# Kernel tuning notes

Measured on AMD Instinct MI355X. Metric: run time of the kernel, lower is better.

Reference implementation:

```python
import jax, jax.numpy as jnp
import numpy as np

BETA = 0.25


def setup_inputs() -> dict:
    key = jax.random.key(0)
    k1, k2 = jax.random.split(key)
    z = jax.random.normal(k1, (16, 64, 64, 64), dtype=jnp.float32)        # [B, e_dim, H, W]
    codebook = jax.random.normal(k2, (2048, 64), dtype=jnp.float32)       # [n_e, e_dim]
    return {"z": z, "codebook": codebook}


def reference(z, codebook):
    B, C, H, W = z.shape
    n_e = codebook.shape[0]
    sg = jax.lax.stop_gradient

    zp = jnp.transpose(z, (0, 2, 3, 1))                # [B, H, W, C]
    zf = zp.reshape(-1, C)                             # [N, C]

    # nearest-code logits (inner product; CE in source is dead code)
    logits = zf @ codebook.T                           # [N, n_e]
    idx = jnp.argmax(logits, axis=1)                   # [N]

    z_q = codebook[idx].reshape(zp.shape)              # [B, H, W, C]

    # commitment + codebook loss (this overwrites the CE loss in the source)
    loss = BETA * jnp.mean((sg(z_q) - zp) ** 2) + jnp.mean((z_q - sg(zp)) ** 2)

    # straight-through estimator
    z_q_st = zp + sg(z_q - zp)

    # perplexity via one-hot mean (scatter-add instead of dense one-hot)
    counts = jnp.zeros((n_e,), dtype=zp.dtype).at[idx].add(1.0)
    e_mean = counts / idx.shape[0]
    perplexity = jnp.exp(-jnp.sum(e_mean * jnp.log(e_mean + 1e-10)))

    indices = idx.reshape(B, H * W).astype(jnp.int32)
    z_q_out = jnp.transpose(z_q_st, (0, 3, 1, 2))      # back to [B, C, H, W]
    return z_q_out, loss, perplexity, indices
```

## Files before the change

kernel.cpp:

```cpp
#include <hip/hip_runtime.h>

#define C_DIM   64
#define HW      4096
#define NROWS   65536
#define N_E     2048
#define N_ELEM  4194304
#define OUT_LOSS_OFF 4194304
#define OUT_PPL_OFF  4194305
#define OUT_IDX_OFF  4194306

#define ROWS_B   128
#define NTILE    (N_E / 16)
#define TILE_U   384

typedef __attribute__((ext_vector_type(8))) short bf16x8;
typedef __attribute__((ext_vector_type(4))) float f32x4;

__device__ __forceinline__ unsigned short f2bf(float f) {
    unsigned u = __float_as_uint(f);
    return (unsigned short)((u + 0x7FFFu + ((u >> 16) & 1u)) >> 16);
}
__device__ __forceinline__ float bf2f(unsigned short b) {
    return __uint_as_float(((unsigned)b) << 16);
}

__global__ __launch_bounds__(256) void vq_prep(
    const float* __restrict__ cb, unsigned short* __restrict__ cbp,
    int* __restrict__ counts, float* __restrict__ loss_accum)
{
    const int u = blockIdx.x * 256 + threadIdx.x;
    if (u < N_E) counts[u] = 0;
    if (u == 0)  *loss_accum = 0.f;
    const int c = u >> 6, k = u & 63;
    const float v = cb[u];
    const unsigned short s1 = f2bf(v);
    const float r1 = v - bf2f(s1);
    const unsigned short s2 = f2bf(r1);
    const float r2 = r1 - bf2f(s2);
    const unsigned short s3 = f2bf(r2);
    const int tile = c >> 4, k2 = k >> 5, kk = k & 31;
    const int lane = (kk >> 3) * 16 + (c & 15), i = kk & 7;
    const int base = ((tile * 3 + 0) * 2 + k2) * 512 + lane * 8 + i;
    cbp[base]        = s1;
    cbp[base + 1024] = s2;
    cbp[base + 2048] = s3;
}

#define M16(A_, B_, C_) __builtin_amdgcn_mfma_f32_16x16x32_bf16((A_), (B_), (C_), 0, 0, 0)

#define PASS8(AA, ACC, NT)                                                      \
    ACC = M16(AA[0], zf[0][NT][0], ACC); ACC = M16(AA[1], zf[0][NT][1], ACC);   \
    ACC = M16(AA[0], zf[1][NT][0], ACC); ACC = M16(AA[1], zf[1][NT][1], ACC);   \
    ACC = M16(AA[2], zf[0][NT][0], ACC); ACC = M16(AA[3], zf[0][NT][1], ACC);   \
    ACC = M16(AA[2], zf[1][NT][0], ACC); ACC = M16(AA[3], zf[1][NT][1], ACC);   \
    ACC = M16(AA[0], zf[2][NT][0], ACC); ACC = M16(AA[1], zf[2][NT][1], ACC);   \
    ACC = M16(AA[4], zf[0][NT][0], ACC); ACC = M16(AA[5], zf[0][NT][1], ACC);   \
    ACC = M16(AA[2], zf[2][NT][0], ACC); ACC = M16(AA[3], zf[2][NT][1], ACC);   \
    ACC = M16(AA[4], zf[1][NT][0], ACC); ACC = M16(AA[5], zf[1][NT][1], ACC);

#define COMPUTE_TILE(T_, AA)                                                    \
    {                                                                           \
        f32x4 acc0 = zero4, acc1 = zero4;                                       \
        PASS8(AA, acc0, 0)                                                      \
        PASS8(AA, acc1, 1)                                                      \
        const int cbase = (T_) * 16 + lg * 4;                                   \
        _Pragma("unroll")                                                       \
        for (int r = 0; r < 4; ++r) {                                           \
            if (acc0[r] > best0) { best0 = acc0[r]; bi0 = cbase + r; }          \
            if (acc1[r] > best1) { best1 = acc1[r]; bi1 = cbase + r; }          \
        }                                                                       \
    }

__global__ __launch_bounds__(256, 2) void vq_mfma(
    const float* __restrict__ z, const float* __restrict__ cb,
    const unsigned short* __restrict__ cbp, float* __restrict__ out,
    int* __restrict__ counts, float* __restrict__ loss_accum)
{
    __shared__ int   sidx[ROWS_B];
    __shared__ float wsum[4];

    const int tid  = threadIdx.x;
    const int lane = tid & 63;
    const int wv   = tid >> 6;
    const int l15  = lane & 15, lg = lane >> 4;
    const int row0 = blockIdx.x * ROWS_B;
    const int b    = row0 >> 12;
    const int hw0  = row0 & 4095;
    const float* zb = z + (size_t)b * C_DIM * HW + hw0;

    bf16x8 zf[3][2][2];
#pragma unroll
    for (int nt = 0; nt < 2; ++nt) {
        const int row_l = wv * 32 + nt * 16 + l15;
#pragma unroll
        for (int k2 = 0; k2 < 2; ++k2) {
#pragma unroll
            for (int i = 0; i < 8; ++i) {
                float v = zb[(size_t)(k2 * 32 + lg * 8 + i) * HW + row_l];
                unsigned short s1 = f2bf(v);
                float r1 = v - bf2f(s1);
                unsigned short s2 = f2bf(r1);
                float r2 = r1 - bf2f(s2);
                zf[0][nt][k2][i] = (short)s1;
                zf[1][nt][k2][i] = (short)s2;
                zf[2][nt][k2][i] = (short)f2bf(r2);
            }
        }
    }

    const bf16x8* cbpf = (const bf16x8*)cbp;
    float best0 = -3.4e38f, best1 = -3.4e38f;
    int   bi0 = 0, bi1 = 0;
    const f32x4 zero4 = {0.f, 0.f, 0.f, 0.f};

    bf16x8 Acur[6], Anxt[6];
#pragma unroll
    for (int f = 0; f < 6; ++f) Acur[f] = cbpf[f * 64 + lane];

#pragma unroll 1
    for (int t = 0; t < NTILE; t += 2) {
#pragma unroll
        for (int f = 0; f < 6; ++f)
            Anxt[f] = cbpf[(size_t)(t + 1) * TILE_U + f * 64 + lane];

        COMPUTE_TILE(t, Acur)

        if (t + 2 < NTILE) {
#pragma unroll
            for (int f = 0; f < 6; ++f)
                Acur[f] = cbpf[(size_t)(t + 2) * TILE_U + f * 64 + lane];
        }

        COMPUTE_TILE(t + 1, Anxt)
    }

#pragma unroll
    for (int off = 16; off <= 32; off <<= 1) {
        float ob; int oi;
        ob = __shfl_xor(best0, off, 64); oi = __shfl_xor(bi0, off, 64);
        if (ob > best0 || (ob == best0 && oi < bi0)) { best0 = ob; bi0 = oi; }
        ob = __shfl_xor(best1, off, 64); oi = __shfl_xor(bi1, off, 64);
        if (ob > best1 || (ob == best1 && oi < bi1)) { best1 = ob; bi1 = oi; }
    }
    if (lane < 32) {
        const int nt = lane >> 4;
        const int row_l = wv * 32 + lane;
        const int ii = (nt == 0) ? bi0 : bi1;
        sidx[row_l] = ii;
        out[OUT_IDX_OFF + row0 + row_l] = (float)ii;
        atomicAdd(&counts[ii], 1);
    }
    __syncthreads();

    float* ob0 = out + (size_t)b * C_DIM * HW + hw0;
    float lsum = 0.f;
#pragma unroll
    for (int j = 0; j < 8; ++j) {
        const int m = j * 256 + tid;
        const int r = m & 127, c4 = m >> 7;
        const float4 q4 = *(const float4*)(cb + (size_t)sidx[r] * C_DIM + c4 * 4);
#pragma unroll
        for (int q = 0; q < 4; ++q) {
            const int c = c4 * 4 + q;
            const float zv = zb[(size_t)c * HW + r];
            const float qv = (q == 0) ? q4.x : (q == 1) ? q4.y : (q == 2) ? q4.z : q4.w;
            const float d = qv - zv;
            lsum += d * d;
            ob0[(size_t)c * HW + r] = zv + d;
        }
    }
    for (int off = 32; off > 0; off >>= 1) lsum += __shfl_down(lsum, off, 64);
    if (lane == 0) wsum[wv] = lsum;
    __syncthreads();
    if (tid == 0)
        atomicAdd(loss_accum, wsum[0] + wsum[1] + wsum[2] + wsum[3]);
}

__global__ __launch_bounds__(256) void vq_finalize(
    const int* __restrict__ counts, const float* __restrict__ loss_accum,
    float* __restrict__ out)
{
    float h = 0.f;
    for (int e = threadIdx.x; e < N_E; e += 256) {
        float em = (float)counts[e] * (1.0f / (float)NROWS);
        h -= em * logf(em + 1e-10f);
    }
    for (int off = 32; off > 0; off >>= 1) h += __shfl_down(h, off, 64);
    __shared__ float hs[4];
    const int lane = threadIdx.x & 63, w = threadIdx.x >> 6;
    if (lane == 0) hs[w] = h;
    __syncthreads();
    if (threadIdx.x == 0) {
        float H = hs[0] + hs[1] + hs[2] + hs[3];
        float m = loss_accum[0] * (1.0f / (float)N_ELEM);
        out[OUT_LOSS_OFF] = 0.25f * m + m;
        out[OUT_PPL_OFF]  = expf(H);
    }
}

extern "C" void kernel_launch(void* const* d_in, const int* in_sizes, int n_in,
                              void* d_out, int out_size, void* d_ws, size_t ws_size,
                              hipStream_t stream)
{
    const float* z  = (const float*)d_in[0];
    const float* cb = (const float*)d_in[1];
    float* out = (float*)d_out;

    int*            counts     = (int*)d_ws;
    float*          loss_accum = (float*)((char*)d_ws + N_E * sizeof(int));
    unsigned short* cbp        = (unsigned short*)((char*)d_ws + 16384);

    vq_prep<<<N_E * C_DIM / 256, 256, 0, stream>>>(cb, cbp, counts, loss_accum);
    vq_mfma<<<NROWS / ROWS_B, 256, 0, stream>>>(z, cb, cbp, out, counts, loss_accum);
    vq_finalize<<<1, 256, 0, stream>>>(counts, loss_accum, out);
}
```

Before: 170.1 us.

## Split codebook across wave pairs and fuse finalize into last block

Each wave now handles 64 rows against half the codebook (1024 codes) instead of 32 rows against all 2048 codes. This doubles reuse of each loaded codebook fragment per MFMA and halves per-wave codebook traffic. The two halves are merged through shared memory. The separate finalize kernel is removed and replaced by a last-block-done atomic counter, saving a launch. In exchange, the z fragments and accumulators use more registers, which may reduce occupancy.

```diff
diff --git a/kernel.cpp b/kernel.cpp
--- a/kernel.cpp
+++ b/kernel.cpp
@@ -10,7 +10,8 @@
 #define OUT_IDX_OFF  4194306
 
 #define ROWS_B   128
-#define NTILE    (N_E / 16)
+#define NBLOCKS  (NROWS / ROWS_B)
+#define NTILE_W  64
 #define TILE_U   384
 
 typedef __attribute__((ext_vector_type(8))) short bf16x8;
@@ -26,11 +27,12 @@
 
 __global__ __launch_bounds__(256) void vq_prep(
     const float* __restrict__ cb, unsigned short* __restrict__ cbp,
-    int* __restrict__ counts, float* __restrict__ loss_accum)
+    int* __restrict__ counts, float* __restrict__ loss_accum,
+    int* __restrict__ done)
 {
     const int u = blockIdx.x * 256 + threadIdx.x;
     if (u < N_E) counts[u] = 0;
-    if (u == 0)  *loss_accum = 0.f;
+    if (u == 0)  { *loss_accum = 0.f; *done = 0; }
     const int c = u >> 6, k = u & 63;
     const float v = cb[u];
     const unsigned short s1 = f2bf(v);
@@ -60,38 +62,50 @@
 
 #define COMPUTE_TILE(T_, AA)                                                    \
     {                                                                           \
-        f32x4 acc0 = zero4, acc1 = zero4;                                       \
+        f32x4 acc0 = zero4, acc1 = zero4, acc2 = zero4, acc3 = zero4;           \
         PASS8(AA, acc0, 0)                                                      \
         PASS8(AA, acc1, 1)                                                      \
-        const int cbase = (T_) * 16 + lg * 4;                                   \
+        PASS8(AA, acc2, 2)                                                      \
+        PASS8(AA, acc3, 3)                                                      \
+        const int cbase = ch * 1024 + (T_) * 16 + lg * 4;                       \
         _Pragma("unroll")                                                       \
         for (int r = 0; r < 4; ++r) {                                           \
             if (acc0[r] > best0) { best0 = acc0[r]; bi0 = cbase + r; }          \
             if (acc1[r] > best1) { best1 = acc1[r]; bi1 = cbase + r; }          \
+            if (acc2[r] > best2) { best2 = acc2[r]; bi2 = cbase + r; }          \
+            if (acc3[r] > best3) { best3 = acc3[r]; bi3 = cbase + r; }          \
         }                                                                       \
     }
 
 __global__ __launch_bounds__(256, 2) void vq_mfma(
     const float* __restrict__ z, const float* __restrict__ cb,
     const unsigned short* __restrict__ cbp, float* __restrict__ out,
-    int* __restrict__ counts, float* __restrict__ loss_accum)
+    int* __restrict__ counts, float* __restrict__ loss_accum,
+    int* __restrict__ done)
 {
+    __shared__ float sbest[2][ROWS_B];
+    __shared__ int   sbi[2][ROWS_B];
     __shared__ int   sidx[ROWS_B];
     __shared__ float wsum[4];
+    __shared__ int   slast;
 
     const int tid  = threadIdx.x;
     const int lane = tid & 63;
     const int wv   = tid >> 6;
     const int l15  = lane & 15, lg = lane >> 4;
+    const int rh   = wv >> 1;
+    const int ch   = wv & 1;
     const int row0 = blockIdx.x * ROWS_B;
     const int b    = row0 >> 12;
     const int hw0  = row0 & 4095;
     const float* zb = z + (size_t)b * C_DIM * HW + hw0;
 
-    bf16x8 zf[3][2][2];
-#pragma unroll
-    for (int nt = 0; nt < 2; ++nt) {
-        const int row_l = wv * 32 + nt * 16 + l15;
+    if (tid == 0) slast = 0;
+
+    bf16x8 zf[3][4][2];
+#pragma unroll
+    for (int nt = 0; nt < 4; ++nt) {
+        const int row_l = rh * 64 + nt * 16 + l15;
 #pragma unroll
         for (int k2 = 0; k2 < 2; ++k2) {
 #pragma unroll
@@ -108,9 +122,9 @@
         }
     }
 
-    const bf16x8* cbpf = (const bf16x8*)cbp;
-    float best0 = -3.4e38f, best1 = -3.4e38f;
-    int   bi0 = 0, bi1 = 0;
+    const bf16x8* cbpf = (const bf16x8*)cbp + (size_t)ch * NTILE_W * TILE_U;
+    float best0 = -3.4e38f, best1 = -3.4e38f, best2 = -3.4e38f, best3 = -3.4e38f;
+    int   bi0 = 0, bi1 = 0, bi2 = 0, bi3 = 0;
     const f32x4 zero4 = {0.f, 0.f, 0.f, 0.f};
 
     bf16x8 Acur[6], Anxt[6];
@@ -118,14 +132,14 @@
     for (int f = 0; f < 6; ++f) Acur[f] = cbpf[f * 64 + lane];
 
 #pragma unroll 1
-    for (int t = 0; t < NTILE; t += 2) {
+    for (int t = 0; t < NTILE_W; t += 2) {
 #pragma unroll
         for (int f = 0; f < 6; ++f)
             Anxt[f] = cbpf[(size_t)(t + 1) * TILE_U + f * 64 + lane];
 
         COMPUTE_TILE(t, Acur)
 
-        if (t + 2 < NTILE) {
+        if (t + 2 < NTILE_W) {
 #pragma unroll
             for (int f = 0; f < 6; ++f)
                 Acur[f] = cbpf[(size_t)(t + 2) * TILE_U + f * 64 + lane];
@@ -141,13 +155,24 @@
         if (ob > best0 || (ob == best0 && oi < bi0)) { best0 = ob; bi0 = oi; }
         ob = __shfl_xor(best1, off, 64); oi = __shfl_xor(bi1, off, 64);
         if (ob > best1 || (ob == best1 && oi < bi1)) { best1 = ob; bi1 = oi; }
-    }
-    if (lane < 32) {
-        const int nt = lane >> 4;
-        const int row_l = wv * 32 + lane;
-        const int ii = (nt == 0) ? bi0 : bi1;
-        sidx[row_l] = ii;
-        out[OUT_IDX_OFF + row0 + row_l] = (float)ii;
+        ob = __shfl_xor(best2, off, 64); oi = __shfl_xor(bi2, off, 64);
+        if (ob > best2 || (ob == best2 && oi < bi2)) { best2 = ob; bi2 = oi; }
+        ob = __shfl_xor(best3, off, 64); oi = __shfl_xor(bi3, off, 64);
+        if (ob > best3 || (ob == best3 && oi < bi3)) { best3 = ob; bi3 = oi; }
+    }
+    {
+        float bb = (lg == 0) ? best0 : (lg == 1) ? best1 : (lg == 2) ? best2 : best3;
+        int   ii = (lg == 0) ? bi0   : (lg == 1) ? bi1   : (lg == 2) ? bi2   : bi3;
+        sbest[ch][rh * 64 + lane] = bb;
+        sbi[ch][rh * 64 + lane]   = ii;
+    }
+    __syncthreads();
+    if (tid < ROWS_B) {
+        float b0 = sbest[0][tid], b1 = sbest[1][tid];
+        int   i0 = sbi[0][tid],   i1 = sbi[1][tid];
+        const int ii = (b1 > b0) ? i1 : i0;
+        sidx[tid] = ii;
+        out[OUT_IDX_OFF + row0 + tid] = (float)ii;
         atomicAdd(&counts[ii], 1);
     }
     __syncthreads();
@@ -172,29 +197,32 @@
     for (int off = 32; off > 0; off >>= 1) lsum += __shfl_down(lsum, off, 64);
     if (lane == 0) wsum[wv] = lsum;
     __syncthreads();
-    if (tid == 0)
+
+    if (tid == 0) {
         atomicAdd(loss_accum, wsum[0] + wsum[1] + wsum[2] + wsum[3]);
-}
-
-__global__ __launch_bounds__(256) void vq_finalize(
-    const int* __restrict__ counts, const float* __restrict__ loss_accum,
-    float* __restrict__ out)
-{
-    float h = 0.f;
-    for (int e = threadIdx.x; e < N_E; e += 256) {
-        float em = (float)counts[e] * (1.0f / (float)NROWS);
-        h -= em * logf(em + 1e-10f);
-    }
-    for (int off = 32; off > 0; off >>= 1) h += __shfl_down(h, off, 64);
-    __shared__ float hs[4];
-    const int lane = threadIdx.x & 63, w = threadIdx.x >> 6;
-    if (lane == 0) hs[w] = h;
-    __syncthreads();
-    if (threadIdx.x == 0) {
-        float H = hs[0] + hs[1] + hs[2] + hs[3];
-        float m = loss_accum[0] * (1.0f / (float)N_ELEM);
-        out[OUT_LOSS_OFF] = 0.25f * m + m;
-        out[OUT_PPL_OFF]  = expf(H);
+        __threadfence();
+        const int tk = atomicAdd(done, 1);
+        if (tk == NBLOCKS - 1) slast = 1;
+    }
+    __syncthreads();
+    if (slast) {
+        __threadfence();
+        float h = 0.f;
+        for (int e = tid; e < N_E; e += 256) {
+            const int cnt = atomicAdd(&counts[e], 0);
+            const float em = (float)cnt * (1.0f / (float)NROWS);
+            h -= em * logf(em + 1e-10f);
+        }
+        for (int off = 32; off > 0; off >>= 1) h += __shfl_down(h, off, 64);
+        if (lane == 0) wsum[wv] = h;
+        __syncthreads();
+        if (tid == 0) {
+            const float H = wsum[0] + wsum[1] + wsum[2] + wsum[3];
+            const float L = atomicAdd(loss_accum, 0.f);
+            const float m = L * (1.0f / (float)N_ELEM);
+            out[OUT_LOSS_OFF] = 0.25f * m + m;
+            out[OUT_PPL_OFF]  = expf(H);
+        }
     }
 }
 
@@ -208,9 +236,9 @@
 
     int*            counts     = (int*)d_ws;
     float*          loss_accum = (float*)((char*)d_ws + N_E * sizeof(int));
+    int*            done       = (int*)((char*)d_ws + N_E * sizeof(int) + 4);
     unsigned short* cbp        = (unsigned short*)((char*)d_ws + 16384);
 
-    vq_prep<<<N_E * C_DIM / 256, 256, 0, stream>>>(cb, cbp, counts, loss_accum);
-    vq_mfma<<<NROWS / ROWS_B, 256, 0, stream>>>(z, cb, cbp, out, counts, loss_accum);
-    vq_finalize<<<1, 256, 0, stream>>>(counts, loss_accum, out);
-}
+    vq_prep<<<N_E * C_DIM / 256, 256, 0, stream>>>(cb, cbp, counts, loss_accum, done);
+    vq_mfma<<<NBLOCKS, 256, 0, stream>>>(z, cb, cbp, out, counts, loss_accum, done);
+}
```

Measured after the change: 174.5 us. 1.03x slower.
